# Kernel tuning notes

Hardware: AMD Instinct MI355X
Metric: run time of the kernel (lower is better)

## Reference

```python
import jax, jax.numpy as jnp
import numpy as np

NUM_HEADS = 8
OUT_FEATS = 64
TOPK_T = 10          # settings['T']
NEG_INF = -9e15

N_NODES = 8192
IN_FEATS = 512
N_EDGES = 262144  # avg degree 32


def setup_inputs() -> dict:
    key = jax.random.key(0)
    k1, k2, k3, k4, k5 = jax.random.split(key, 5)
    feat = jax.random.normal(k1, (N_NODES, IN_FEATS), jnp.float32)
    # xavier-ish scale for the fc weight [H*D, in_feats]
    fc_weight = jax.random.normal(k2, (NUM_HEADS * OUT_FEATS, IN_FEATS), jnp.float32) * 0.05
    trans_m = jax.random.uniform(k3, (N_EDGES,), jnp.float32)
    src = jax.random.randint(k4, (N_EDGES,), 0, N_NODES, dtype=jnp.int32)
    dst = jax.random.randint(k5, (N_EDGES,), 0, N_NODES, dtype=jnp.int32)
    return {"feat": feat, "fc_weight": fc_weight, "trans_m": trans_m, "src": src, "dst": dst}


def reference(feat, fc_weight, trans_m, src, dst):
    N = feat.shape[0]
    # fc projection -> [N, H, D]
    feat_src = (feat @ fc_weight.T).reshape(N, NUM_HEADS, OUT_FEATS)
    # per-edge per-head dot-product score (SDDMM; same math as the gathered NxN matmul)
    fs, fd = feat_src[src], feat_src[dst]           # [Ne, H, D]
    e = jnp.einsum('ehd,ehd->eh', fs, fd)           # [Ne, H]
    # sparse attn values = sum over heads of e * trans_m, scattered into dense [N, N]
    vals = (e * trans_m[:, None]).sum(-1)           # [Ne]
    attn_dense = jnp.zeros((N, N), feat.dtype).at[src, dst].add(vals)
    # topk mask per row: threshold = clamp(kth largest, min=0); below -> -9e15
    thresh = jnp.maximum(jax.lax.top_k(attn_dense, TOPK_T)[0][:, -1], 0.0)  # [N]
    masked = jnp.where(attn_dense < thresh[:, None], NEG_INF, attn_dense)
    # attn = masked.T ; gather attn[src, dst] == masked[dst, src]; mask edges where < -100
    cond = masked[dst, src] < -100.0                # [Ne]
    e = jnp.where(cond[:, None], NEG_INF, e)
    # edge_softmax over incoming edges of each dst node
    emax = jax.ops.segment_max(e, dst, num_segments=N)        # [N, H]
    e_exp = jnp.exp(e - emax[dst])                            # [Ne, H]
    esum = jax.ops.segment_sum(e_exp, dst, num_segments=N)    # [N, H]
    a = e_exp / esum[dst]                                     # [Ne, H]
    # u_mul_e + sum aggregation: rst[v] = sum_{(u,v) in E} a * feat_src[u]
    rst = jax.ops.segment_sum(a[:, :, None] * fs, dst, num_segments=N)  # [N, H, D]
    return rst
```

## Files before the change

kernel.cpp:

```cpp
#include <hip/hip_runtime.h>
#include <hip/hip_bf16.h>
#include <math.h>

#define N_NODES 8192
#define IN_FEATS 512
#define N_EDGES 262144
#define NUM_HEADS 8
#define OUT_FEATS 64
#define HD (NUM_HEADS * OUT_FEATS)
#define TOPK 10
#define NEG_INF -9e15f
#define MAXD 128
#define EID_MASK 0x3FFFF

__device__ __forceinline__ int swz(int row, int k4) {
  return k4 ^ (4 * (((row & 7) ^ ((row >> 3) & 7)) & 7));
}

__global__ __launch_bounds__(512, 2) void gemm_nt(const float* __restrict__ A,
                                                  const float* __restrict__ B,
                                                  float* __restrict__ C,
                                                  ushort* __restrict__ C16) {
  __shared__ char smem[65536];
  int tid = threadIdx.x;
  int sub = tid >> 8;
  int stid = tid & 255;
  int tx = stid & 15, ty = stid >> 4;
  int brow = blockIdx.x * 128, bcol = blockIdx.y * 128;
  int kbase = sub * 256;

  float (*Asub)[32] = (float(*)[32])(smem + sub * 16384);
  float (*Bsub)[32] = (float(*)[32])(smem + 32768 + sub * 16384);

  int sr = stid >> 1;
  int skc = (stid & 1) * 8;
  const float* gA = A + (size_t)(brow + sr) * IN_FEATS + kbase + skc;
  const float* gB = B + (size_t)(bcol + sr) * IN_FEATS + kbase + skc;
  int w0 = swz(sr, skc), w1 = swz(sr, skc + 4);

  float acc[8][8];
#pragma unroll
  for (int i = 0; i < 8; i++)
#pragma unroll
    for (int j = 0; j < 8; j++) acc[i][j] = 0.f;

  float4 ra0 = *(const float4*)gA;
  float4 ra1 = *(const float4*)(gA + 4);
  float4 rb0 = *(const float4*)gB;
  float4 rb1 = *(const float4*)(gB + 4);

  const int NT = 16;
  for (int t = 0; t < NT; ++t) {
    __syncthreads();
    *(float4*)&Asub[sr][w0] = ra0; *(float4*)&Asub[sr][w1] = ra1;
    *(float4*)&Bsub[sr][w0] = rb0; *(float4*)&Bsub[sr][w1] = rb1;
    if (t + 1 < NT) {
      const float* pA = gA + (t + 1) * 16;
      const float* pB = gB + (t + 1) * 16;
      ra0 = *(const float4*)pA; ra1 = *(const float4*)(pA + 4);
      rb0 = *(const float4*)pB; rb1 = *(const float4*)(pB + 4);
    }
    __syncthreads();
#pragma unroll
    for (int g = 0; g < 4; ++g) {
      float4 av[8], bv[8];
#pragma unroll
      for (int i = 0; i < 8; i++) {
        int r = ty * 8 + i;
        av[i] = *(const float4*)&Asub[r][swz(r, g * 4)];
      }
#pragma unroll
      for (int j = 0; j < 8; j++) {
        int c = tx * 8 + j;
        bv[j] = *(const float4*)&Bsub[c][swz(c, g * 4)];
      }
#pragma unroll
      for (int i = 0; i < 8; i++)
#pragma unroll
        for (int j = 0; j < 8; j++) {
          acc[i][j] = fmaf(av[i].x, bv[j].x, acc[i][j]);
          acc[i][j] = fmaf(av[i].y, bv[j].y, acc[i][j]);
          acc[i][j] = fmaf(av[i].z, bv[j].z, acc[i][j]);
          acc[i][j] = fmaf(av[i].w, bv[j].w, acc[i][j]);
        }
    }
  }

  float (*xch)[33] = (float(*)[33])smem;
  __syncthreads();
#pragma unroll
  for (int r = 0; r < 2; ++r) {
    if (sub == 1) {
#pragma unroll
      for (int k = 0; k < 32; ++k) {
        int idx = r * 32 + k;
        xch[stid][k] = acc[idx >> 3][idx & 7];
      }
    }
    __syncthreads();
    if (sub == 0) {
#pragma unroll
      for (int k = 0; k < 32; ++k) {
        int idx = r * 32 + k;
        acc[idx >> 3][idx & 7] += xch[stid][k];
      }
    }
    __syncthreads();
  }

  if (sub == 0) {
#pragma unroll
    for (int i = 0; i < 8; i++) {
      int row = brow + ty * 8 + i;
      float* cp = C + (size_t)row * HD + bcol + tx * 8;
      *(float4*)cp = make_float4(acc[i][0], acc[i][1], acc[i][2], acc[i][3]);
      *(float4*)(cp + 4) = make_float4(acc[i][4], acc[i][5], acc[i][6], acc[i][7]);
      ushort u[8];
#pragma unroll
      for (int j = 0; j < 8; j++) u[j] = __bfloat16_as_ushort(__float2bfloat16(acc[i][j]));
      uint4 q;
      q.x = (unsigned)u[0] | ((unsigned)u[1] << 16);
      q.y = (unsigned)u[2] | ((unsigned)u[3] << 16);
      q.z = (unsigned)u[4] | ((unsigned)u[5] << 16);
      q.w = (unsigned)u[6] | ((unsigned)u[7] << 16);
      *(uint4*)(C16 + (size_t)row * HD + bcol + tx * 8) = q;
    }
  }
}

__global__ __launch_bounds__(256) void histo(const int* __restrict__ src, const int* __restrict__ dst,
                                             int* __restrict__ cnt_s, int* __restrict__ cnt_d) {
  int e = blockIdx.x * blockDim.x + threadIdx.x;
  if (e < N_EDGES) {
    atomicAdd(&cnt_s[src[e]], 1);
    atomicAdd(&cnt_d[dst[e]], 1);
  }
}

__global__ __launch_bounds__(1024) void scan2(const int* __restrict__ cnt_s, const int* __restrict__ cnt_d,
                                              int* __restrict__ rp_s, int* __restrict__ rp_d) {
  __shared__ int ls[1024];
  const int* cnt = blockIdx.x ? cnt_d : cnt_s;
  int* rp = blockIdx.x ? rp_d : rp_s;
  int t = threadIdx.x;
  int base = t * 8;
  int v[8]; int s = 0;
#pragma unroll
  for (int i = 0; i < 8; i++) { v[i] = cnt[base + i]; s += v[i]; }
  ls[t] = s;
  __syncthreads();
  for (int off = 1; off < 1024; off <<= 1) {
    int x = (t >= off) ? ls[t - off] : 0;
    __syncthreads();
    ls[t] += x;
    __syncthreads();
  }
  int excl = (t == 0) ? 0 : ls[t - 1];
#pragma unroll
  for (int i = 0; i < 8; i++) { rp[base + i] = excl; excl += v[i]; }
  if (t == 1023) rp[N_NODES] = excl;
}

__global__ __launch_bounds__(256) void scatter_csr(const int* __restrict__ src, const int* __restrict__ dst,
                                                   const int* __restrict__ rp_s, const int* __restrict__ rp_d,
                                                   int* __restrict__ fill_s, int* __restrict__ fill_d,
                                                   int* __restrict__ cs, int* __restrict__ cd) {
  int e = blockIdx.x * blockDim.x + threadIdx.x;
  if (e < N_EDGES) {
    int p = rp_s[src[e]] + atomicAdd(&fill_s[src[e]], 1);
    cs[p] = e;
    int q = rp_d[dst[e]] + atomicAdd(&fill_d[dst[e]], 1);
    cd[q] = e;
  }
}

__global__ __launch_bounds__(256) void sort_rows_bitonic(const int* __restrict__ rp_s,
                                                         const int* __restrict__ rp_d,
                                                         const int* __restrict__ dst,
                                                         int* __restrict__ cs, int* __restrict__ cd,
                                                         int* __restrict__ keys_s) {
  int wave = (blockIdx.x * blockDim.x + threadIdx.x) >> 6;
  int lane = threadIdx.x & 63;
  bool is_s = wave < N_NODES;
  int r = is_s ? wave : wave - N_NODES;
  const int* rp = is_s ? rp_s : rp_d;
  int b = rp[r], e2 = rp[r + 1];
  int len = e2 - b; if (len > 128) len = 128;

  int x0 = 0x7FFFFFFF, x1 = 0x7FFFFFFF;
  if (lane < len) {
    int e = is_s ? cs[b + lane] : cd[b + lane];
    x0 = is_s ? ((dst[e] << 18) | e) : e;
  }
  if (lane + 64 < len) {
    int e = is_s ? cs[b + lane + 64] : cd[b + lane + 64];
    x1 = is_s ? ((dst[e] << 18) | e) : e;
  }

  for (int s = 2; s <= 64; s <<= 1) {
    bool asc1 = ((64 & s) == 0);
    for (int d = s >> 1; d >= 1; d >>= 1) {
      {
        int y = __shfl_xor(x0, d);
        bool keepmin = (((lane & d) == 0) == ((lane & s) == 0));
        x0 = keepmin ? min(x0, y) : max(x0, y);
      }
      {
        int y = __shfl_xor(x1, d);
        bool asc = asc1 ? ((lane & s) == 0) : false;
        bool keepmin = (((lane & d) == 0) == asc);
        x1 = keepmin ? min(x1, y) : max(x1, y);
      }
    }
  }
  { int lo = min(x0, x1), hi = max(x0, x1); x0 = lo; x1 = hi; }
  for (int d = 32; d >= 1; d >>= 1) {
    {
      int y = __shfl_xor(x0, d);
      bool keepmin = ((lane & d) == 0);
      x0 = keepmin ? min(x0, y) : max(x0, y);
    }
    {
      int y = __shfl_xor(x1, d);
      bool keepmin = ((lane & d) == 0);
      x1 = keepmin ? min(x1, y) : max(x1, y);
    }
  }

  if (lane < len) {
    if (is_s) { cs[b + lane] = x0 & EID_MASK; keys_s[b + lane] = x0; }
    else cd[b + lane] = x0;
  }
  if (lane + 64 < len) {
    if (is_s) { cs[b + lane + 64] = x1 & EID_MASK; keys_s[b + lane + 64] = x1; }
    else cd[b + lane + 64] = x1;
  }
}

__global__ __launch_bounds__(256) void edge_scores_row(const float* __restrict__ fsrc,
                                                       const int* __restrict__ dst,
                                                       const float* __restrict__ trans,
                                                       const int* __restrict__ rp_s,
                                                       const int* __restrict__ cs,
                                                       float* __restrict__ escore, float* __restrict__ val) {
  int wave = (blockIdx.x * blockDim.x + threadIdx.x) >> 6;
  int lane = threadIdx.x & 63;
  if (wave >= N_NODES) return;
  int b = rp_s[wave], e2 = rp_s[wave + 1];
  if (b == e2) return;
  const float4* ps = (const float4*)(fsrc + (size_t)wave * HD) + lane * 2;
  float4 s0 = ps[0], s1 = ps[1];
  int head = lane >> 3;
  bool leader = (lane & 7) == 0;
  for (int i = b; i < e2; i += 4) {
    int n = e2 - i; if (n > 4) n = 4;
    int ee[4];
    float4 d0[4], d1[4];
#pragma unroll
    for (int k = 0; k < 4; k++) {
      int idx = (k < n) ? (i + k) : i;
      int e = cs[idx];
      ee[k] = e;
      const float4* pd = (const float4*)(fsrc + (size_t)dst[e] * HD) + lane * 2;
      d0[k] = pd[0];
      d1[k] = pd[1];
    }
#pragma unroll
    for (int k = 0; k < 4; k++) {
      if (k < n) {
        float dot = s0.x * d0[k].x + s0.y * d0[k].y + s0.z * d0[k].z + s0.w * d0[k].w
                  + s1.x * d1[k].x + s1.y * d1[k].y + s1.z * d1[k].z + s1.w * d1[k].w;
        dot += __shfl_xor(dot, 1);
        dot += __shfl_xor(dot, 2);
        dot += __shfl_xor(dot, 4);
        int e = ee[k];
        if (leader) escore[(size_t)e * 8 + head] = dot;
        float x = leader ? dot * trans[e] : 0.f;
        x += __shfl_xor(x, 8);
        x += __shfl_xor(x, 16);
        x += __shfl_xor(x, 32);
        if (lane == 0) val[e] = x;
      }
    }
  }
}

__global__ __launch_bounds__(256) void topk_wave(const int* __restrict__ rp_s,
                                                 const int* __restrict__ keys_s,
                                                 const float* __restrict__ val,
                                                 float* __restrict__ aval,
                                                 float* __restrict__ thresh) {
  int wave = (blockIdx.x * blockDim.x + threadIdx.x) >> 6;
  int lane = threadIdx.x & 63;
  if (wave >= N_NODES) return;
  int b = rp_s[wave], e2 = rp_s[wave + 1];
  int len = e2 - b; if (len > 128) len = 128;
  float c[2];
#pragma unroll
  for (int k = 0; k < 2; k++) {
    int i = lane + 64 * k;
    float cv = 0.f;
    if (i < len) {
      int key = keys_s[b + i];
      int d = key >> 18;
      int prevd = (i == 0) ? -1 : (keys_s[b + i - 1] >> 18);
      if (d != prevd) {
        float s = val[key & EID_MASK];
        for (int j = i + 1; j < len; j++) {
          int kj = keys_s[b + j];
          if ((kj >> 18) != d) break;
          s += val[kj & EID_MASK];
        }
        cv = s;
        aval[b + i] = s;
      } else {
        aval[b + i] = 0.f;
      }
    }
    c[k] = cv;
  }
  float t10 = 0.f;
  for (int t = 0; t < 10; t++) {
    float m = fmaxf(c[0], c[1]);
#pragma unroll
    for (int off = 1; off < 64; off <<= 1) m = fmaxf(m, __shfl_xor(m, off));
    if (m <= 0.f) { t10 = 0.f; break; }
    t10 = m;
    if (t == 9) break;
    unsigned long long b0 = __ballot(c[0] == m);
    if (b0) {
      int l = __ffsll(b0) - 1;
      if (lane == l) c[0] = -1e30f;
    } else {
      unsigned long long b1 = __ballot(c[1] == m);
      int l = __ffsll(b1) - 1;
      if (lane == l) c[1] = -1e30f;
    }
  }
  if (lane == 0) thresh[wave] = fmaxf(t10, 0.f);
}

__global__ __launch_bounds__(256) void cond_edges(const int* __restrict__ src, const int* __restrict__ dst,
                                                  const int* __restrict__ rp_s,
                                                  const int* __restrict__ keys_s,
                                                  const float* __restrict__ aval,
                                                  const float* __restrict__ thresh,
                                                  unsigned char* __restrict__ cond) {
  int e = blockIdx.x * blockDim.x + threadIdx.x;
  if (e >= N_EDGES) return;
  int s = src[e], d = dst[e];
  int lo = rp_s[d], hi = rp_s[d + 1];
  int end = hi;
  int target = s << 18;
  while (lo < hi) {
    int mid = (lo + hi) >> 1;
    if (keys_s[mid] < target) lo = mid + 1; else hi = mid;
  }
  float a = 0.f;
  if (lo < end && (keys_s[lo] >> 18) == s) a = aval[lo];
  cond[e] = (a < thresh[d]) ? 1 : 0;
}

__global__ __launch_bounds__(256) void dst_softmax_agg(const int* __restrict__ rp_d, const int* __restrict__ cd,
                                                       const int* __restrict__ src,
                                                       const unsigned char* __restrict__ cond,
                                                       const float* __restrict__ escore,
                                                       const ushort* __restrict__ fsrc16,
                                                       float* __restrict__ out) {
  __shared__ float p_lds[4][MAXD * 9];
  __shared__ int u_lds[4][MAXD];
  int w = threadIdx.x >> 6;
  int lane = threadIdx.x & 63;
  int v = blockIdx.x * 4 + w;
  float* pl = p_lds[w];
  int* ul = u_lds[w];
  int rb = rp_d[v], re = rp_d[v + 1];
  int d = re - rb;
  if (d > MAXD) d = MAXD;

  float sc[2][8];
  float m[8];
#pragma unroll
  for (int h = 0; h < 8; h++) m[h] = -3.0e38f;

#pragma unroll
  for (int k = 0; k < 2; k++) {
    int il = lane + 64 * k;
    if (il < d) {
      int ei = cd[rb + il];
      int u = src[ei];
      ul[il] = u;
      bool cmask = cond[ei] != 0;
      const float* sp = escore + (size_t)ei * 8;
      float4 s0 = *(const float4*)sp;
      float4 s1 = *(const float4*)(sp + 4);
      float ss[8] = {s0.x, s0.y, s0.z, s0.w, s1.x, s1.y, s1.z, s1.w};
#pragma unroll
      for (int h = 0; h < 8; h++) {
        float x = cmask ? NEG_INF : ss[h];
        sc[k][h] = x;
        m[h] = fmaxf(m[h], x);
      }
    } else {
#pragma unroll
      for (int h = 0; h < 8; h++) sc[k][h] = -3.0e38f;
    }
  }
#pragma unroll
  for (int off = 1; off < 64; off <<= 1)
#pragma unroll
    for (int h = 0; h < 8; h++) m[h] = fmaxf(m[h], __shfl_xor(m[h], off));

  float z[8];
#pragma unroll
  for (int h = 0; h < 8; h++) z[h] = 0.f;
#pragma unroll
  for (int k = 0; k < 2; k++) {
    int il = lane + 64 * k;
    if (il < d) {
#pragma unroll
      for (int h = 0; h < 8; h++) {
        float p = expf(sc[k][h] - m[h]);
        z[h] += p;
        pl[il * 9 + h] = p;
      }
    }
  }
#pragma unroll
  for (int off = 1; off < 64; off <<= 1)
#pragma unroll
    for (int h = 0; h < 8; h++) z[h] += __shfl_xor(z[h], off);

  int myh = lane >> 3;
  float zh = 0.f;
#pragma unroll
  for (int h = 0; h < 8; h++) zh = (h == myh) ? z[h] : zh;
  float invZ = (d > 0) ? (1.0f / zh) : 0.f;

  __syncthreads();

  float a0[8], a1[8], a2[8], a3[8];
#pragma unroll
  for (int j = 0; j < 8; j++) { a0[j] = 0.f; a1[j] = 0.f; a2[j] = 0.f; a3[j] = 0.f; }
  int i = 0;
  for (; i + 4 <= d; i += 4) {
    float w0 = pl[(i + 0) * 9 + myh] * invZ;
    float w1 = pl[(i + 1) * 9 + myh] * invZ;
    float w2 = pl[(i + 2) * 9 + myh] * invZ;
    float w3 = pl[(i + 3) * 9 + myh] * invZ;
    uint4 q0 = *(const uint4*)(fsrc16 + (size_t)ul[i + 0] * HD + lane * 8);
    uint4 q1 = *(const uint4*)(fsrc16 + (size_t)ul[i + 1] * HD + lane * 8);
    uint4 q2 = *(const uint4*)(fsrc16 + (size_t)ul[i + 2] * HD + lane * 8);
    uint4 q3 = *(const uint4*)(fsrc16 + (size_t)ul[i + 3] * HD + lane * 8);
    a0[0] = fmaf(w0, __uint_as_float(q0.x << 16), a0[0]);
    a0[1] = fmaf(w0, __uint_as_float(q0.x & 0xFFFF0000u), a0[1]);
    a0[2] = fmaf(w0, __uint_as_float(q0.y << 16), a0[2]);
    a0[3] = fmaf(w0, __uint_as_float(q0.y & 0xFFFF0000u), a0[3]);
    a0[4] = fmaf(w0, __uint_as_float(q0.z << 16), a0[4]);
    a0[5] = fmaf(w0, __uint_as_float(q0.z & 0xFFFF0000u), a0[5]);
    a0[6] = fmaf(w0, __uint_as_float(q0.w << 16), a0[6]);
    a0[7] = fmaf(w0, __uint_as_float(q0.w & 0xFFFF0000u), a0[7]);
    a1[0] = fmaf(w1, __uint_as_float(q1.x << 16), a1[0]);
    a1[1] = fmaf(w1, __uint_as_float(q1.x & 0xFFFF0000u), a1[1]);
    a1[2] = fmaf(w1, __uint_as_float(q1.y << 16), a1[2]);
    a1[3] = fmaf(w1, __uint_as_float(q1.y & 0xFFFF0000u), a1[3]);
    a1[4] = fmaf(w1, __uint_as_float(q1.z << 16), a1[4]);
    a1[5] = fmaf(w1, __uint_as_float(q1.z & 0xFFFF0000u), a1[5]);
    a1[6] = fmaf(w1, __uint_as_float(q1.w << 16), a1[6]);
    a1[7] = fmaf(w1, __uint_as_float(q1.w & 0xFFFF0000u), a1[7]);
    a2[0] = fmaf(w2, __uint_as_float(q2.x << 16), a2[0]);
    a2[1] = fmaf(w2, __uint_as_float(q2.x & 0xFFFF0000u), a2[1]);
    a2[2] = fmaf(w2, __uint_as_float(q2.y << 16), a2[2]);
    a2[3] = fmaf(w2, __uint_as_float(q2.y & 0xFFFF0000u), a2[3]);
    a2[4] = fmaf(w2, __uint_as_float(q2.z << 16), a2[4]);
    a2[5] = fmaf(w2, __uint_as_float(q2.z & 0xFFFF0000u), a2[5]);
    a2[6] = fmaf(w2, __uint_as_float(q2.w << 16), a2[6]);
    a2[7] = fmaf(w2, __uint_as_float(q2.w & 0xFFFF0000u), a2[7]);
    a3[0] = fmaf(w3, __uint_as_float(q3.x << 16), a3[0]);
    a3[1] = fmaf(w3, __uint_as_float(q3.x & 0xFFFF0000u), a3[1]);
    a3[2] = fmaf(w3, __uint_as_float(q3.y << 16), a3[2]);
    a3[3] = fmaf(w3, __uint_as_float(q3.y & 0xFFFF0000u), a3[3]);
    a3[4] = fmaf(w3, __uint_as_float(q3.z << 16), a3[4]);
    a3[5] = fmaf(w3, __uint_as_float(q3.z & 0xFFFF0000u), a3[5]);
    a3[6] = fmaf(w3, __uint_as_float(q3.w << 16), a3[6]);
    a3[7] = fmaf(w3, __uint_as_float(q3.w & 0xFFFF0000u), a3[7]);
  }
  for (; i < d; ++i) {
    float ww = pl[i * 9 + myh] * invZ;
    uint4 q = *(const uint4*)(fsrc16 + (size_t)ul[i] * HD + lane * 8);
    a0[0] = fmaf(ww, __uint_as_float(q.x << 16), a0[0]);
    a0[1] = fmaf(ww, __uint_as_float(q.x & 0xFFFF0000u), a0[1]);
    a0[2] = fmaf(ww, __uint_as_float(q.y << 16), a0[2]);
    a0[3] = fmaf(ww, __uint_as_float(q.y & 0xFFFF0000u), a0[3]);
    a0[4] = fmaf(ww, __uint_as_float(q.z << 16), a0[4]);
    a0[5] = fmaf(ww, __uint_as_float(q.z & 0xFFFF0000u), a0[5]);
    a0[6] = fmaf(ww, __uint_as_float(q.w << 16), a0[6]);
    a0[7] = fmaf(ww, __uint_as_float(q.w & 0xFFFF0000u), a0[7]);
  }
  float* op = out + (size_t)v * HD + lane * 8;
  *(float4*)op = make_float4((a0[0] + a1[0]) + (a2[0] + a3[0]),
                             (a0[1] + a1[1]) + (a2[1] + a3[1]),
                             (a0[2] + a1[2]) + (a2[2] + a3[2]),
                             (a0[3] + a1[3]) + (a2[3] + a3[3]));
  *(float4*)(op + 4) = make_float4((a0[4] + a1[4]) + (a2[4] + a3[4]),
                                   (a0[5] + a1[5]) + (a2[5] + a3[5]),
                                   (a0[6] + a1[6]) + (a2[6] + a3[6]),
                                   (a0[7] + a1[7]) + (a2[7] + a3[7]));
}

extern "C" void kernel_launch(void* const* d_in, const int* in_sizes, int n_in,
                              void* d_out, int out_size, void* d_ws, size_t ws_size,
                              hipStream_t stream) {
  const float* feat = (const float*)d_in[0];
  const float* fcw = (const float*)d_in[1];
  const float* trans = (const float*)d_in[2];
  const int* src = (const int*)d_in[3];
  const int* dst = (const int*)d_in[4];
  float* out = (float*)d_out;

  char* ws = (char*)d_ws;
  size_t off = 0;
  auto alloc = [&](size_t bytes) -> void* {
    size_t o = off;
    off = (off + bytes + 255) & ~(size_t)255;
    return (void*)(ws + o);
  };
  float* fsrc = (float*)alloc((size_t)N_NODES * HD * 4);
  ushort* fsrc16 = (ushort*)alloc((size_t)N_NODES * HD * 2);
  float* escore = (float*)alloc((size_t)N_EDGES * 8 * 4);
  float* val = (float*)alloc((size_t)N_EDGES * 4);
  int* cnt = (int*)alloc((size_t)4 * N_NODES * 4);
  int* rp_s = (int*)alloc((size_t)(N_NODES + 1) * 4);
  int* rp_d = (int*)alloc((size_t)(N_NODES + 1) * 4);
  int* cs = (int*)alloc((size_t)N_EDGES * 4);
  int* cd = (int*)alloc((size_t)N_EDGES * 4);
  int* keys_s = (int*)alloc((size_t)N_EDGES * 4);
  float* aval = (float*)alloc((size_t)N_EDGES * 4);
  float* thresh = (float*)alloc((size_t)N_NODES * 4);
  unsigned char* cond = (unsigned char*)alloc((size_t)N_EDGES);
  if (off > ws_size) return;

  int* cnt_s = cnt;
  int* cnt_d = cnt + N_NODES;
  int* fill_s = cnt + 2 * N_NODES;
  int* fill_d = cnt + 3 * N_NODES;

  hipMemsetAsync(cnt, 0, (size_t)4 * N_NODES * 4, stream);
  histo<<<N_EDGES / 256, 256, 0, stream>>>(src, dst, cnt_s, cnt_d);
  scan2<<<2, 1024, 0, stream>>>(cnt_s, cnt_d, rp_s, rp_d);
  scatter_csr<<<N_EDGES / 256, 256, 0, stream>>>(src, dst, rp_s, rp_d, fill_s, fill_d, cs, cd);
  sort_rows_bitonic<<<(2 * N_NODES * 64) / 256, 256, 0, stream>>>(rp_s, rp_d, dst, cs, cd, keys_s);
  gemm_nt<<<dim3(N_NODES / 128, HD / 128), 512, 0, stream>>>(feat, fcw, fsrc, fsrc16);
  edge_scores_row<<<(N_NODES * 64) / 256, 256, 0, stream>>>(fsrc, dst, trans, rp_s, cs, escore, val);
  topk_wave<<<(N_NODES * 64) / 256, 256, 0, stream>>>(rp_s, keys_s, val, aval, thresh);
  cond_edges<<<N_EDGES / 256, 256, 0, stream>>>(src, dst, rp_s, keys_s, aval, thresh, cond);
  dst_softmax_agg<<<N_NODES / 4, 256, 0, stream>>>(rp_d, cd, src, cond, escore, fsrc16, out);
}
```

Baseline: 256.1 us.

## Split edge score rows into destination-range groups for cache locality

Edges in each source row are already sorted by destination, so the bitonic sort kernel now also records offsets splitting each row into 8 groups by the top bits of the destination id. The edge-score kernel launches one block per (group, 4 rows), so blocks sharing a group gather destination features from a narrower slice of fsrc, which should improve L2 hit rates on the gather. It costs extra launch blocks (many nearly empty), a small offset table, and repeated loading of the source row feature per group.

```diff
diff --git a/kernel.cpp b/kernel.cpp
--- a/kernel.cpp
+++ b/kernel.cpp
@@ -12,6 +12,7 @@
 #define NEG_INF -9e15f
 #define MAXD 128
 #define EID_MASK 0x3FFFF
+#define NGRP 8
 
 __device__ __forceinline__ int swz(int row, int k4) {
   return k4 ^ (4 * (((row & 7) ^ ((row >> 3) & 7)) & 7));
@@ -178,7 +179,8 @@
                                                          const int* __restrict__ rp_d,
                                                          const int* __restrict__ dst,
                                                          int* __restrict__ cs, int* __restrict__ cd,
-                                                         int* __restrict__ keys_s) {
+                                                         int* __restrict__ keys_s,
+                                                         int* __restrict__ grp_off) {
   int wave = (blockIdx.x * blockDim.x + threadIdx.x) >> 6;
   int lane = threadIdx.x & 63;
   bool is_s = wave < N_NODES;
@@ -235,20 +237,38 @@
     if (is_s) { cs[b + lane + 64] = x1 & EID_MASK; keys_s[b + lane + 64] = x1; }
     else cd[b + lane + 64] = x1;
   }
-}
-
-__global__ __launch_bounds__(256) void edge_scores_row(const float* __restrict__ fsrc,
-                                                       const int* __restrict__ dst,
-                                                       const float* __restrict__ trans,
-                                                       const int* __restrict__ rp_s,
-                                                       const int* __restrict__ cs,
-                                                       float* __restrict__ escore, float* __restrict__ val) {
-  int wave = (blockIdx.x * blockDim.x + threadIdx.x) >> 6;
+
+  if (is_s) {
+    int g0 = (lane < len) ? (x0 >> 28) : 8;
+    int g1 = (lane + 64 < len) ? (x1 >> 28) : 8;
+    int g0p = __shfl_up(g0, 1);
+    if (lane == 0) g0p = -1;
+    int g1p = __shfl_up(g1, 1);
+    int g0last = __shfl(g0, 63);
+    if (lane == 0) g1p = g0last;
+    for (int gg = g0p + 1; gg <= g0 && gg <= 7; ++gg) grp_off[r * NGRP + gg] = b + lane;
+    for (int gg = g1p + 1; gg <= g1 && gg <= 7; ++gg) grp_off[r * NGRP + gg] = b + lane + 64;
+    if (lane == 63) {
+      for (int gg = g1 + 1; gg <= 7; ++gg) grp_off[r * NGRP + gg] = b + 128;
+    }
+  }
+}
+
+__global__ __launch_bounds__(256, 4) void edge_scores_grp(const float* __restrict__ fsrc,
+                                                          const int* __restrict__ dst,
+                                                          const float* __restrict__ trans,
+                                                          const int* __restrict__ rp_s,
+                                                          const int* __restrict__ cs,
+                                                          const int* __restrict__ grp_off,
+                                                          float* __restrict__ escore,
+                                                          float* __restrict__ val) {
+  int g = blockIdx.x & 7;
+  int r = (blockIdx.x >> 3) * 4 + (threadIdx.x >> 6);
   int lane = threadIdx.x & 63;
-  if (wave >= N_NODES) return;
-  int b = rp_s[wave], e2 = rp_s[wave + 1];
-  if (b == e2) return;
-  const float4* ps = (const float4*)(fsrc + (size_t)wave * HD) + lane * 2;
+  int b = grp_off[r * NGRP + g];
+  int e2 = (g == 7) ? rp_s[r + 1] : grp_off[r * NGRP + g + 1];
+  if (b >= e2) return;
+  const float4* ps = (const float4*)(fsrc + (size_t)r * HD) + lane * 2;
   float4 s0 = ps[0], s1 = ps[1];
   int head = lane >> 3;
   bool leader = (lane & 7) == 0;
@@ -537,6 +557,7 @@
   int* keys_s = (int*)alloc((size_t)N_EDGES * 4);
   float* aval = (float*)alloc((size_t)N_EDGES * 4);
   float* thresh = (float*)alloc((size_t)N_NODES * 4);
+  int* grp_off = (int*)alloc((size_t)N_NODES * NGRP * 4);
   unsigned char* cond = (unsigned char*)alloc((size_t)N_EDGES);
   if (off > ws_size) return;
 
@@ -549,9 +570,9 @@
   histo<<<N_EDGES / 256, 256, 0, stream>>>(src, dst, cnt_s, cnt_d);
   scan2<<<2, 1024, 0, stream>>>(cnt_s, cnt_d, rp_s, rp_d);
   scatter_csr<<<N_EDGES / 256, 256, 0, stream>>>(src, dst, rp_s, rp_d, fill_s, fill_d, cs, cd);
-  sort_rows_bitonic<<<(2 * N_NODES * 64) / 256, 256, 0, stream>>>(rp_s, rp_d, dst, cs, cd, keys_s);
+  sort_rows_bitonic<<<(2 * N_NODES * 64) / 256, 256, 0, stream>>>(rp_s, rp_d, dst, cs, cd, keys_s, grp_off);
   gemm_nt<<<dim3(N_NODES / 128, HD / 128), 512, 0, stream>>>(feat, fcw, fsrc, fsrc16);
-  edge_scores_row<<<(N_NODES * 64) / 256, 256, 0, stream>>>(fsrc, dst, trans, rp_s, cs, escore, val);
+  edge_scores_grp<<<NGRP * (N_NODES / 4), 256, 0, stream>>>(fsrc, dst, trans, rp_s, cs, grp_off, escore, val);
   topk_wave<<<(N_NODES * 64) / 256, 256, 0, stream>>>(rp_s, keys_s, val, aval, thresh);
   cond_edges<<<N_EDGES / 256, 256, 0, stream>>>(src, dst, rp_s, keys_s, aval, thresh, cond);
   dst_softmax_agg<<<N_NODES / 4, 256, 0, stream>>>(rp_d, cd, src, cond, escore, fsrc16, out);
```

After: 252.8 us. No clear change (-1.3%).
